# Kernel tuning notes

Hardware: AMD Instinct MI355X
Metric: run time of the kernel (lower is better)

## Reference

```python
import jax, jax.numpy as jnp
from jax import lax
import numpy as np

UNITS = 400
FEAT = 3
B, T = 64, 512


def _lstm_layer(x, Wx, Wh, pi, pf, po, b):
    """Peephole LSTM (Graves 2013). x: [B,T,D] -> [B,T,U]."""
    Bsz = x.shape[0]
    U = Wh.shape[0]
    # Precompute input projections for all timesteps: [B,T,4U]
    xproj = jnp.einsum('btd,dk->btk', x, Wx) + b
    xs = jnp.swapaxes(xproj, 0, 1)  # [T,B,4U]

    def step(carry, xp):
        h, c = carry
        z = xp + h @ Wh  # [B,4U]
        zi, zf, zg, zo = jnp.split(z, 4, axis=-1)
        i = jax.nn.sigmoid(zi + pi * c)
        f = jax.nn.sigmoid(zf + pf * c)
        g = jnp.tanh(zg)
        c_new = f * c + i * g
        o = jax.nn.sigmoid(zo + po * c_new)
        h_new = o * jnp.tanh(c_new)
        return (h_new, c_new), h_new

    init = (jnp.zeros((Bsz, U), x.dtype), jnp.zeros((Bsz, U), x.dtype))
    _, hs = lax.scan(step, init, xs)
    return jnp.swapaxes(hs, 0, 1)  # [B,T,U]


def setup_inputs() -> dict:
    key = jax.random.key(0)
    ks = jax.random.split(key, 32)
    ki = iter(range(32))
    s = 0.05
    d = {'x': jax.random.normal(ks[next(ki)], (B, T, FEAT), jnp.float32)}
    in_dims = [FEAT, UNITS, UNITS]
    for l, din in enumerate(in_dims):
        d[f'Wx{l}'] = jax.random.normal(ks[next(ki)], (din, 4 * UNITS), jnp.float32) * s
        d[f'Wh{l}'] = jax.random.normal(ks[next(ki)], (UNITS, 4 * UNITS), jnp.float32) * s
        d[f'pi{l}'] = jax.random.normal(ks[next(ki)], (UNITS,), jnp.float32) * s
        d[f'pf{l}'] = jax.random.normal(ks[next(ki)], (UNITS,), jnp.float32) * s
        d[f'po{l}'] = jax.random.normal(ks[next(ki)], (UNITS,), jnp.float32) * s
        d[f'b{l}'] = jnp.zeros((4 * UNITS,), jnp.float32)
    d['Wd'] = jax.random.normal(ks[next(ki)], (UNITS, FEAT), jnp.float32) * s
    d['bd'] = jnp.zeros((FEAT,), jnp.float32)
    return d


def reference(x, Wx0, Wh0, pi0, pf0, po0, b0,
              Wx1, Wh1, pi1, pf1, po1, b1,
              Wx2, Wh2, pi2, pf2, po2, b2,
              Wd, bd):
    h = _lstm_layer(x, Wx0, Wh0, pi0, pf0, po0, b0)
    h = _lstm_layer(h, Wx1, Wh1, pi1, pf1, po1, b1)
    h = _lstm_layer(h, Wx2, Wh2, pi2, pf2, po2, b2)
    return h @ Wd + bd  # [B,T,FEAT]
```

## Files before the change

kernel.cpp:

```cpp
#include <hip/hip_runtime.h>
#include <math.h>

#define B64   64
#define TT    512
#define U400  400
#define G1600 1600
#define NBPL  80
#define UPB   5
#define NCOL  (4 * UPB)
#define NW    8
#define NTHR  512
#define NBLK  (3 * NBPL)

__device__ __forceinline__ float ldg_c(const float* p) {
  return __hip_atomic_load(p, __ATOMIC_RELAXED, __HIP_MEMORY_SCOPE_AGENT);
}
__device__ __forceinline__ void stg_c(float* p, float v) {
  __hip_atomic_store(p, v, __ATOMIC_RELAXED, __HIP_MEMORY_SCOPE_AGENT);
}
__device__ __forceinline__ int adl(const unsigned* p) {
  return (int)__hip_atomic_load(p, __ATOMIC_RELAXED, __HIP_MEMORY_SCOPE_AGENT);
}

__global__ void xpose_x_k(const float* __restrict__ x, float* __restrict__ xT) {
  int idx = blockIdx.x * 256 + threadIdx.x;
  if (idx < B64 * TT * 3) {
    int d = idx % 3;
    int t = (idx / 3) % TT;
    int b = idx / (3 * TT);
    xT[(t * 3 + d) * B64 + b] = x[idx];
  }
}

__global__ void transpose_k(const float* __restrict__ in, float* __restrict__ out,
                            int R, int C) {
  __shared__ float tile[32][33];
  int bx = blockIdx.x * 32, by = blockIdx.y * 32;
  int tx = threadIdx.x, ty = threadIdx.y;
  #pragma unroll
  for (int i = ty; i < 32; i += 8) {
    int r = by + i, c = bx + tx;
    if (r < R && c < C) tile[i][tx] = in[(size_t)r * C + c];
  }
  __syncthreads();
  #pragma unroll
  for (int i = ty; i < 32; i += 8) {
    int r = bx + i, c = by + tx;
    if (r < C && c < R) out[(size_t)r * R + c] = tile[tx][i];
  }
}

__device__ __forceinline__ void issue10(const float* __restrict__ base, int lane,
                                        float (&buf)[10]) {
  #pragma unroll
  for (int i = 0; i < 10; ++i)
    buf[i] = ldg_c(base + (size_t)i * B64 + lane);
}

__device__ __forceinline__ void cons10(const float (&buf)[10], int koff,
                                       const float* const (&wrow)[NCOL],
                                       float (&acc)[NCOL]) {
  #pragma unroll
  for (int i = 0; i < 10; ++i) {
    const float a = buf[i];
    #pragma unroll
    for (int c = 0; c < NCOL; ++c) acc[c] += a * wrow[c][koff + i];
  }
}

__device__ __forceinline__ void gemm100(const float* __restrict__ aslab, int lane,
                                        const float* const (&wrow)[NCOL],
                                        float (&acc)[NCOL]) {
  float aA[10], aB[10];
  issue10(aslab +  0 * B64, lane, aA);
  issue10(aslab + 10 * B64, lane, aB);
  cons10(aA,  0, wrow, acc); issue10(aslab + 20 * B64, lane, aA);
  cons10(aB, 10, wrow, acc); issue10(aslab + 30 * B64, lane, aB);
  cons10(aA, 20, wrow, acc); issue10(aslab + 40 * B64, lane, aA);
  cons10(aB, 30, wrow, acc); issue10(aslab + 50 * B64, lane, aB);
  cons10(aA, 40, wrow, acc); issue10(aslab + 60 * B64, lane, aA);
  cons10(aB, 50, wrow, acc); issue10(aslab + 70 * B64, lane, aB);
  cons10(aA, 60, wrow, acc); issue10(aslab + 80 * B64, lane, aA);
  cons10(aB, 70, wrow, acc); issue10(aslab + 90 * B64, lane, aB);
  cons10(aA, 80, wrow, acc);
  cons10(aB, 90, wrow, acc);
}

__device__ __forceinline__ void gemm50(const float* __restrict__ aslab, int lane,
                                       const float* const (&wrow)[NCOL],
                                       float (&acc)[NCOL]) {
  float aA[10], aB[10];
  issue10(aslab +  0 * B64, lane, aA);
  issue10(aslab + 10 * B64, lane, aB);
  cons10(aA,  0, wrow, acc); issue10(aslab + 20 * B64, lane, aA);
  cons10(aB, 10, wrow, acc); issue10(aslab + 30 * B64, lane, aB);
  cons10(aA, 20, wrow, acc); issue10(aslab + 40 * B64, lane, aA);
  cons10(aB, 30, wrow, acc);
  cons10(aA, 40, wrow, acc);
}

struct ScanP {
  const float *xT0, *Wx0;
  const float *WxT1, *WxT2;
  const float *WhT0, *WhT1, *WhT2;
  const float *b0, *b1, *b2;
  const float *pi0, *pi1, *pi2;
  const float *pf0, *pf1, *pf2;
  const float *po0, *po1, *po2;
  float *h0r, *h1r;
  float *h2;
  unsigned *syn;
};

#define CNT(l)    (p.syn + (l) * 32)
#define ROOT(l)   (p.syn + (3 + (l)) * 32)
#define GRP(l, g) (p.syn + (6 + (l) * 8 + (g)) * 32)

__launch_bounds__(NTHR, 1)
__global__ void lstm_scan_k(ScanP p) {
  const int l    = blockIdx.x / NBPL;
  const int u0   = (blockIdx.x % NBPL) * UPB;
  const int grp  = (blockIdx.x % NBPL) / 10;
  const int lane = threadIdx.x & 63;
  const int kq   = __builtin_amdgcn_readfirstlane(threadIdx.x >> 6);

  __shared__ float zs[NW][NCOL][B64];

  const float* WhT  = (l == 0) ? p.WhT0 : (l == 1 ? p.WhT1 : p.WhT2);
  const float* WxT  = (l == 1) ? p.WxT1 : p.WxT2;
  const float* bias = (l == 0) ? p.b0  : (l == 1 ? p.b1  : p.b2);
  const float* pi   = (l == 0) ? p.pi0 : (l == 1 ? p.pi1 : p.pi2);
  const float* pf   = (l == 0) ? p.pf0 : (l == 1 ? p.pf1 : p.pf2);
  const float* po   = (l == 0) ? p.po0 : (l == 1 ? p.po1 : p.po2);
  const float* prevb = (l == 1) ? p.h0r : p.h1r;
  float* ownb = (l == 0) ? p.h0r : (l == 1 ? p.h1r : p.h2);
  const int ownmask = (l == 2) ? (TT - 1) : 7;

  const float* wb; int k0, isH;
  if (l == 0)      { wb = WhT; k0 = kq * 50;        isH = 1; }
  else if (kq < 4) { wb = WxT; k0 = kq * 100;       isH = 0; }
  else             { wb = WhT; k0 = (kq - 4) * 100; isH = 1; }

  const float* wrow[NCOL];
  #pragma unroll
  for (int g = 0; g < 4; ++g)
    #pragma unroll
    for (int uu = 0; uu < UPB; ++uu)
      wrow[g * UPB + uu] = wb + (size_t)(g * U400 + u0 + uu) * U400 + k0;

  float creg = 0.f;

  for (int t = 0; t < TT; ++t) {
    if (threadIdx.x == 0) {
      while (adl(CNT(l)) < t) __builtin_amdgcn_s_sleep(4);
      if (l > 0)
        while (adl(CNT(l - 1)) < t + 1) __builtin_amdgcn_s_sleep(4);
      if (l < 2)
        while (adl(CNT(l + 1)) < t - 7) __builtin_amdgcn_s_sleep(4);
    }
    __syncthreads();

    {
      float acc[NCOL];
      #pragma unroll
      for (int c = 0; c < NCOL; ++c) acc[c] = 0.f;

      if (!(isH && t == 0)) {
        const float* aslab = isH
            ? ownb  + (size_t)((t - 1) & ownmask) * (U400 * B64) + (size_t)k0 * B64
            : prevb + (size_t)(t & 7)             * (U400 * B64) + (size_t)k0 * B64;
        if (l == 0) gemm50(aslab, lane, wrow, acc);
        else        gemm100(aslab, lane, wrow, acc);
      }
      #pragma unroll
      for (int c = 0; c < NCOL; ++c) zs[kq][c][lane] = acc[c];
    }
    __syncthreads();

    if (threadIdx.x < UPB * B64) {
      const int uu = threadIdx.x >> 6;
      const int b  = lane;
      const int u  = u0 + uu;
      float z0 = bias[0 * U400 + u], z1 = bias[1 * U400 + u];
      float z2 = bias[2 * U400 + u], z3 = bias[3 * U400 + u];
      #pragma unroll
      for (int w = 0; w < NW; ++w) {
        z0 += zs[w][0 * UPB + uu][b];
        z1 += zs[w][1 * UPB + uu][b];
        z2 += zs[w][2 * UPB + uu][b];
        z3 += zs[w][3 * UPB + uu][b];
      }
      if (l == 0) {
        #pragma unroll
        for (int dd = 0; dd < 3; ++dd) {
          float xv = p.xT0[(t * 3 + dd) * B64 + b];
          z0 += xv * p.Wx0[dd * G1600 + 0 * U400 + u];
          z1 += xv * p.Wx0[dd * G1600 + 1 * U400 + u];
          z2 += xv * p.Wx0[dd * G1600 + 2 * U400 + u];
          z3 += xv * p.Wx0[dd * G1600 + 3 * U400 + u];
        }
      }
      float cp = creg;
      float ig = 1.f / (1.f + expf(-(z0 + pi[u] * cp)));
      float fg = 1.f / (1.f + expf(-(z1 + pf[u] * cp)));
      float gg = tanhf(z2);
      float cn = fg * cp + ig * gg;
      float og = 1.f / (1.f + expf(-(z3 + po[u] * cn)));
      creg = cn;
      float h = og * tanhf(cn);
      stg_c(&ownb[(size_t)(t & ownmask) * (U400 * B64) + (size_t)u * B64 + b], h);
    }

    __syncthreads();

    if (threadIdx.x == 0) {
      unsigned go = __hip_atomic_fetch_add(GRP(l, grp), 1u, __ATOMIC_RELAXED,
                                           __HIP_MEMORY_SCOPE_AGENT);
      if (go == (unsigned)((t + 1) * 10 - 1)) {
        unsigned ro = __hip_atomic_fetch_add(ROOT(l), 1u, __ATOMIC_RELAXED,
                                             __HIP_MEMORY_SCOPE_AGENT);
        if (ro == (unsigned)((t + 1) * 8 - 1))
          __hip_atomic_store(CNT(l), (unsigned)(t + 1), __ATOMIC_RELAXED,
                             __HIP_MEMORY_SCOPE_AGENT);
      }
    }
  }
}

__launch_bounds__(256)
__global__ void dense_k(const float* __restrict__ h2, const float* __restrict__ Wd,
                        const float* __restrict__ bd, float* __restrict__ out) {
  int wid  = blockIdx.x * 4 + (threadIdx.x >> 6);
  int lane = threadIdx.x & 63;
  int t = wid / 3, f = wid - t * 3;
  if (t >= TT) return;
  float acc = bd[f];
  const float* hrow = h2 + (size_t)t * U400 * B64 + lane;
  #pragma unroll 4
  for (int u = 0; u < U400; ++u) acc += hrow[(size_t)u * B64] * Wd[u * 3 + f];
  out[((size_t)lane * TT + t) * 3 + f] = acc;
}

extern "C" void kernel_launch(void* const* d_in, const int* in_sizes, int n_in,
                              void* d_out, int out_size, void* d_ws, size_t ws_size,
                              hipStream_t stream) {
  const float* x   = (const float*)d_in[0];
  const float* Wx0 = (const float*)d_in[1];
  const float* Wh0 = (const float*)d_in[2];
  const float* pi0 = (const float*)d_in[3];
  const float* pf0 = (const float*)d_in[4];
  const float* po0 = (const float*)d_in[5];
  const float* b0  = (const float*)d_in[6];
  const float* Wx1 = (const float*)d_in[7];
  const float* Wh1 = (const float*)d_in[8];
  const float* pi1 = (const float*)d_in[9];
  const float* pf1 = (const float*)d_in[10];
  const float* po1 = (const float*)d_in[11];
  const float* b1  = (const float*)d_in[12];
  const float* Wx2 = (const float*)d_in[13];
  const float* Wh2 = (const float*)d_in[14];
  const float* pi2 = (const float*)d_in[15];
  const float* pf2 = (const float*)d_in[16];
  const float* po2 = (const float*)d_in[17];
  const float* b2  = (const float*)d_in[18];
  const float* Wd  = (const float*)d_in[19];
  const float* bd  = (const float*)d_in[20];

  float* ws   = (float*)d_ws;
  float* xT0  = ws;
  float* WhT0 = xT0  + 98304;
  float* WhT1 = WhT0 + 640000;
  float* WhT2 = WhT1 + 640000;
  float* WxT1 = WhT2 + 640000;
  float* WxT2 = WxT1 + 640000;
  float* h0r  = WxT2 + 640000;
  float* h1r  = h0r  + 204800;
  float* h2   = h1r  + 204800;
  unsigned* syn = (unsigned*)(h2 + 13107200);

  hipMemsetAsync(syn, 0, 30 * 128, stream);

  hipLaunchKernelGGL(xpose_x_k, dim3(384), dim3(256), 0, stream, x, xT0);

  dim3 tb(32, 8);
  dim3 tg((G1600 + 31) / 32, (U400 + 31) / 32);
  hipLaunchKernelGGL(transpose_k, tg, tb, 0, stream, Wh0, WhT0, U400, G1600);
  hipLaunchKernelGGL(transpose_k, tg, tb, 0, stream, Wh1, WhT1, U400, G1600);
  hipLaunchKernelGGL(transpose_k, tg, tb, 0, stream, Wh2, WhT2, U400, G1600);
  hipLaunchKernelGGL(transpose_k, tg, tb, 0, stream, Wx1, WxT1, U400, G1600);
  hipLaunchKernelGGL(transpose_k, tg, tb, 0, stream, Wx2, WxT2, U400, G1600);

  ScanP hp;
  hp.xT0 = xT0;  hp.Wx0 = Wx0;
  hp.WxT1 = WxT1; hp.WxT2 = WxT2;
  hp.WhT0 = WhT0; hp.WhT1 = WhT1; hp.WhT2 = WhT2;
  hp.b0 = b0; hp.b1 = b1; hp.b2 = b2;
  hp.pi0 = pi0; hp.pi1 = pi1; hp.pi2 = pi2;
  hp.pf0 = pf0; hp.pf1 = pf1; hp.pf2 = pf2;
  hp.po0 = po0; hp.po1 = po1; hp.po2 = po2;
  hp.h0r = h0r; hp.h1r = h1r; hp.h2 = h2;
  hp.syn = syn;

  void* args[] = { &hp };
  hipLaunchCooperativeKernel((void*)lstm_scan_k, dim3(NBLK), dim3(NTHR),
                             args, 0, stream);

  hipLaunchKernelGGL(dense_k, dim3(384), dim3(256), 0, stream, h2, Wd, bd,
                     (float*)d_out);
}
```

Baseline: 19.61 ms.

## Stage recurrent activations into LDS via async global_load_lds double buffering

Per-lane agent-scope atomic loads of the h/x activation slabs are replaced with direct global-to-LDS 16-byte async copies, staged in 20-row chunks and double-buffered per wave with explicit vmcnt waits. Layer 0's K split is rebalanced into 60- and 40-row pieces so the chunk size divides evenly. The aim is fewer, wider memory instructions and a deeper load/compute overlap. It adds about 80KB of LDS and depends on hand-written waitcnt ordering. It also drops the atomic-load semantics used for cross-block visibility, which may affect coherence.

```diff
diff --git a/kernel.cpp b/kernel.cpp
--- a/kernel.cpp
+++ b/kernel.cpp
@@ -1,5 +1,6 @@
 #include <hip/hip_runtime.h>
 #include <math.h>
+#include <stdint.h>
 
 #define B64   64
 #define TT    512
@@ -50,53 +51,36 @@
   }
 }
 
-__device__ __forceinline__ void issue10(const float* __restrict__ base, int lane,
-                                        float (&buf)[10]) {
-  #pragma unroll
-  for (int i = 0; i < 10; ++i)
-    buf[i] = ldg_c(base + (size_t)i * B64 + lane);
-}
-
-__device__ __forceinline__ void cons10(const float (&buf)[10], int koff,
-                                       const float* const (&wrow)[NCOL],
-                                       float (&acc)[NCOL]) {
-  #pragma unroll
-  for (int i = 0; i < 10; ++i) {
-    const float a = buf[i];
+__device__ __forceinline__ void stage_chunk(const float* g, float (*buf)[B64]) {
+  #pragma unroll
+  for (int j = 0; j < 5; ++j)
+    __builtin_amdgcn_global_load_lds(
+        (const __attribute__((address_space(1))) void*)(g + j * 4 * B64),
+        (__attribute__((address_space(3))) void*)(&buf[4 * j][0]),
+        16, 0, 16 );
+}
+
+template <int NCH>
+__device__ __forceinline__ void gemm_lds(const float* __restrict__ aslab, int lane,
+                                         float (*stg)[20][B64],
+                                         const float* const (&wrow)[NCOL],
+                                         float (&acc)[NCOL]) {
+  const float* g = aslab + ((lane >> 4) << 6) + ((lane & 15) << 2);
+  stage_chunk(g, stg[0]);
+  if (NCH > 1) stage_chunk(g + 20 * B64, stg[1]);
+  #pragma unroll
+  for (int c = 0; c < NCH; ++c) {
+    if (c + 1 < NCH) asm volatile("s_waitcnt vmcnt(5)" ::: "memory");
+    else             asm volatile("s_waitcnt vmcnt(0)" ::: "memory");
     #pragma unroll
-    for (int c = 0; c < NCOL; ++c) acc[c] += a * wrow[c][koff + i];
-  }
-}
-
-__device__ __forceinline__ void gemm100(const float* __restrict__ aslab, int lane,
-                                        const float* const (&wrow)[NCOL],
-                                        float (&acc)[NCOL]) {
-  float aA[10], aB[10];
-  issue10(aslab +  0 * B64, lane, aA);
-  issue10(aslab + 10 * B64, lane, aB);
-  cons10(aA,  0, wrow, acc); issue10(aslab + 20 * B64, lane, aA);
-  cons10(aB, 10, wrow, acc); issue10(aslab + 30 * B64, lane, aB);
-  cons10(aA, 20, wrow, acc); issue10(aslab + 40 * B64, lane, aA);
-  cons10(aB, 30, wrow, acc); issue10(aslab + 50 * B64, lane, aB);
-  cons10(aA, 40, wrow, acc); issue10(aslab + 60 * B64, lane, aA);
-  cons10(aB, 50, wrow, acc); issue10(aslab + 70 * B64, lane, aB);
-  cons10(aA, 60, wrow, acc); issue10(aslab + 80 * B64, lane, aA);
-  cons10(aB, 70, wrow, acc); issue10(aslab + 90 * B64, lane, aB);
-  cons10(aA, 80, wrow, acc);
-  cons10(aB, 90, wrow, acc);
-}
-
-__device__ __forceinline__ void gemm50(const float* __restrict__ aslab, int lane,
-                                       const float* const (&wrow)[NCOL],
-                                       float (&acc)[NCOL]) {
-  float aA[10], aB[10];
-  issue10(aslab +  0 * B64, lane, aA);
-  issue10(aslab + 10 * B64, lane, aB);
-  cons10(aA,  0, wrow, acc); issue10(aslab + 20 * B64, lane, aA);
-  cons10(aB, 10, wrow, acc); issue10(aslab + 30 * B64, lane, aB);
-  cons10(aA, 20, wrow, acc); issue10(aslab + 40 * B64, lane, aA);
-  cons10(aB, 30, wrow, acc);
-  cons10(aA, 40, wrow, acc);
+    for (int i = 0; i < 20; ++i) {
+      const float a = stg[c & 1][i][lane];
+      #pragma unroll
+      for (int cc = 0; cc < NCOL; ++cc) acc[cc] += a * wrow[cc][c * 20 + i];
+    }
+    if (c + 2 < NCH)
+      stage_chunk(g + (c + 2) * 20 * B64, stg[c & 1]);
+  }
 }
 
 struct ScanP {
@@ -125,6 +109,7 @@
   const int kq   = __builtin_amdgcn_readfirstlane(threadIdx.x >> 6);
 
   __shared__ float zs[NW][NCOL][B64];
+  __shared__ float stage[NW][2][20][B64];
 
   const float* WhT  = (l == 0) ? p.WhT0 : (l == 1 ? p.WhT1 : p.WhT2);
   const float* WxT  = (l == 1) ? p.WxT1 : p.WxT2;
@@ -136,10 +121,16 @@
   float* ownb = (l == 0) ? p.h0r : (l == 1 ? p.h1r : p.h2);
   const int ownmask = (l == 2) ? (TT - 1) : 7;
 
-  const float* wb; int k0, isH;
-  if (l == 0)      { wb = WhT; k0 = kq * 50;        isH = 1; }
-  else if (kq < 4) { wb = WxT; k0 = kq * 100;       isH = 0; }
-  else             { wb = WhT; k0 = (kq - 4) * 100; isH = 1; }
+  const float* wb; int k0, isH, nch;
+  if (l == 0) {
+    wb = WhT; isH = 1;
+    if (kq < 4) { k0 = kq * 60;             nch = 3; }
+    else        { k0 = 240 + (kq - 4) * 40; nch = 2; }
+  } else if (kq < 4) {
+    wb = WxT; isH = 0; k0 = kq * 100;       nch = 5;
+  } else {
+    wb = WhT; isH = 1; k0 = (kq - 4) * 100; nch = 5;
+  }
 
   const float* wrow[NCOL];
   #pragma unroll
@@ -169,8 +160,9 @@
         const float* aslab = isH
             ? ownb  + (size_t)((t - 1) & ownmask) * (U400 * B64) + (size_t)k0 * B64
             : prevb + (size_t)(t & 7)             * (U400 * B64) + (size_t)k0 * B64;
-        if (l == 0) gemm50(aslab, lane, wrow, acc);
-        else        gemm100(aslab, lane, wrow, acc);
+        if (nch == 5)      gemm_lds<5>(aslab, lane, stage[kq], wrow, acc);
+        else if (nch == 3) gemm_lds<3>(aslab, lane, stage[kq], wrow, acc);
+        else               gemm_lds<2>(aslab, lane, stage[kq], wrow, acc);
       }
       #pragma unroll
       for (int c = 0; c < NCOL; ++c) zs[kq][c][lane] = acc[c];
```

Result: no change. 19.77 ms (+0.8%).
